# Performance work log

Hardware: AMD Instinct MI355X
Metric: run time of the kernel (lower is better)

The kernel has to match this reference:

```python
import jax, jax.numpy as jnp
import numpy as np

ITERS = 10
EPS = 1e-6
TEMPERATURE = 1.0


def setup_inputs() -> dict:
    key = jax.random.key(0)
    S, E = 524288, 64
    logits = jax.random.normal(key, (S, E), dtype=jnp.float32)
    return {"logits": logits, "top_k": 2}


def reference(logits, top_k):
    s, e = logits.shape
    scores = (logits / TEMPERATURE).astype(jnp.float32)
    scores = scores - jnp.max(scores, axis=-1, keepdims=True)
    q = jnp.exp(scores)
    col_target = float(s) / float(max(e, 1))

    def body(q, _):
        q = q / (jnp.sum(q, axis=1, keepdims=True) + EPS)
        q = q / (jnp.sum(q, axis=0, keepdims=True) + EPS) * col_target
        return q, None

    q, _ = jax.lax.scan(body, q, None, length=ITERS)
    q = q / (jnp.sum(q, axis=1, keepdims=True) + EPS)
    vals, idx = jax.lax.top_k(q, top_k)
    w = vals / (jnp.sum(vals, axis=-1, keepdims=True) + EPS)
    return idx.astype(jnp.int64), w.astype(logits.dtype)
```

## Files before the change

kernel.cpp:

```cpp
#include <hip/hip_runtime.h>
#include <math.h>

#define EPS 1e-6f
#define NE 64
#define TPB 1024
#define WPB 16
#define NBLK 256
#define NWAVES (NBLK * WPB)
#define ITERS 10
#define PF 4

template <int ctrl>
__device__ __forceinline__ float dppf(float x) {
    return __int_as_float(__builtin_amdgcn_update_dpp(
        0, __float_as_int(x), ctrl, 0xf, 0xf, true));
}
template <int ctrl>
__device__ __forceinline__ int dppi(int x) {
    return __builtin_amdgcn_update_dpp(0, x, ctrl, 0xf, 0xf, true);
}

__device__ __forceinline__ float group16_sum(float v) {
    v += dppf<0xB1>(v);
    v += dppf<0x4E>(v);
    v += dppf<0x141>(v);
    v += dppf<0x140>(v);
    return v;
}

#define ARGMAX_STEP(CTRL)                                      \
    {                                                          \
        float ov = dppf<CTRL>(v);                              \
        int oi = dppi<CTRL>(i);                                \
        if (ov > v || (ov == v && oi < i)) { v = ov; i = oi; } \
    }

__device__ __forceinline__ void group16_argmax(float& v, int& i) {
    ARGMAX_STEP(0xB1)
    ARGMAX_STEP(0x4E)
    ARGMAX_STEP(0x141)
    ARGMAX_STEP(0x140)
}

template <bool FIRST>
__global__ __launch_bounds__(TPB) void sink_pass(
    const float4* __restrict__ logits4, float* __restrict__ r,
    float* __restrict__ c, float* __restrict__ Pblk,
    unsigned* __restrict__ counters, int nquads, float col_target, int it) {
    const int tid = threadIdx.x;
    const int lane = tid & 63;
    const int wib = tid >> 6;
    const int g = lane >> 4;
    const int h = lane & 15;
    const int qpw = nquads / NWAVES;
    const int qbase = (blockIdx.x * WPB + wib) * qpw;

    float4 c4;
    if (FIRST) c4 = make_float4(1.f, 1.f, 1.f, 1.f);
    else       c4 = ((const float4*)c)[h];

    const float4* lp = logits4 + (size_t)qbase * 64 + lane;

    float4 buf[PF];
    float rbuf[PF];
#pragma unroll
    for (int p = 0; p < PF; ++p) buf[p] = lp[(size_t)p * 64];
    if (!FIRST) {
#pragma unroll
        for (int p = 0; p < PF; ++p) rbuf[p] = r[(qbase + p) * 4 + g];
    }

    float4 pacc = {0.f, 0.f, 0.f, 0.f};
    const int nb = qpw / PF;
    for (int b = 0; b < nb; ++b) {
        float4 cur[PF];
        float rcur[PF];
#pragma unroll
        for (int p = 0; p < PF; ++p) {
            cur[p] = buf[p];
            if (!FIRST) rcur[p] = rbuf[p];
        }
        if (b + 1 < nb) {
            const float4* np = lp + (size_t)(b + 1) * PF * 64;
#pragma unroll
            for (int p = 0; p < PF; ++p) buf[p] = np[(size_t)p * 64];
            if (!FIRST) {
#pragma unroll
                for (int p = 0; p < PF; ++p)
                    rbuf[p] = r[(qbase + (b + 1) * PF + p) * 4 + g];
            }
        }
#pragma unroll
        for (int p = 0; p < PF; ++p) {
            float4 q;
            q.x = __expf(cur[p].x); q.y = __expf(cur[p].y);
            q.z = __expf(cur[p].z); q.w = __expf(cur[p].w);
            float s = q.x * c4.x + q.y * c4.y + q.z * c4.z + q.w * c4.w;
            s = group16_sum(s);
            float rold = FIRST ? 1.0f : rcur[p];
            float rnew = rold / (rold * s + EPS);
            int row = (qbase + b * PF + p) * 4 + g;
            if (h == 0) r[row] = rnew;
            pacc.x += q.x * rnew; pacc.y += q.y * rnew;
            pacc.z += q.z * rnew; pacc.w += q.w * rnew;
        }
    }

    __shared__ float4 plds[WPB][64];
    __shared__ int lastflag;
    plds[wib][lane] = pacc;
    __syncthreads();
    if (tid < NE) {
        int j = tid, hh = j >> 2, kk = j & 3;
        float t = 0.f;
#pragma unroll
        for (int w = 0; w < WPB; ++w)
#pragma unroll
            for (int gg = 0; gg < 4; ++gg)
                t += ((const float*)&plds[w][gg * 16 + hh])[kk];
        Pblk[blockIdx.x * NE + j] = t;
        __threadfence();
    }
    __syncthreads();
    if (tid == 0) {
        unsigned old = atomicAdd(&counters[it], 1u);
        lastflag = (old == (unsigned)(NBLK - 1));
    }
    __syncthreads();

    if (lastflag) {
        __threadfence();
        float* s_red = (float*)plds;
        const int j = tid & 63;
        const int chunk = tid >> 6;
        float t = 0.f;
        int b0 = chunk * (NBLK / 16);
        for (int b = b0; b < b0 + NBLK / 16; ++b) t += Pblk[b * NE + j];
        __syncthreads();
        s_red[chunk * NE + j] = t;
        __syncthreads();
        if (tid < NE) {
            float P = 0.f;
#pragma unroll
            for (int k = 0; k < 16; ++k) P += s_red[k * NE + tid];
            float cj = FIRST ? 1.0f : c[tid];
            c[tid] = cj * col_target / (cj * P + EPS);
            __threadfence();
        }
    }
}

__global__ __launch_bounds__(TPB) void sink_final(
    const float4* __restrict__ logits4, const float* __restrict__ r,
    const float* __restrict__ c, float2* __restrict__ oidx,
    float2* __restrict__ ow, int nquads) {
    const int tid = threadIdx.x;
    const int lane = tid & 63;
    const int wib = tid >> 6;
    const int g = lane >> 4;
    const int h = lane & 15;
    const int base_col = h * 4;
    const int qpw = nquads / NWAVES;
    const int qbase = (blockIdx.x * WPB + wib) * qpw;

    const float4 c4 = ((const float4*)c)[h];
    const float4* lp = logits4 + (size_t)qbase * 64 + lane;

    float4 buf[PF];
    float rbuf[PF];
#pragma unroll
    for (int p = 0; p < PF; ++p) buf[p] = lp[(size_t)p * 64];
#pragma unroll
    for (int p = 0; p < PF; ++p) rbuf[p] = r[(qbase + p) * 4 + g];

    const int nb = qpw / PF;
    for (int b = 0; b < nb; ++b) {
        float4 cur[PF];
        float rcur[PF];
#pragma unroll
        for (int p = 0; p < PF; ++p) { cur[p] = buf[p]; rcur[p] = rbuf[p]; }
        if (b + 1 < nb) {
            const float4* np = lp + (size_t)(b + 1) * PF * 64;
#pragma unroll
            for (int p = 0; p < PF; ++p) buf[p] = np[(size_t)p * 64];
#pragma unroll
            for (int p = 0; p < PF; ++p)
                rbuf[p] = r[(qbase + (b + 1) * PF + p) * 4 + g];
        }
#pragma unroll
        for (int p = 0; p < PF; ++p) {
            float4 u;
            u.x = __expf(cur[p].x) * c4.x; u.y = __expf(cur[p].y) * c4.y;
            u.z = __expf(cur[p].z) * c4.z; u.w = __expf(cur[p].w) * c4.w;
            float s = group16_sum(u.x + u.y + u.z + u.w);
            float rold = rcur[p];
            float rnew = rold / (rold * s + EPS);
            float4 val;
            val.x = u.x * rnew; val.y = u.y * rnew;
            val.z = u.z * rnew; val.w = u.w * rnew;

            float v = val.x; int i = base_col;
            if (val.y > v) { v = val.y; i = base_col + 1; }
            if (val.z > v) { v = val.z; i = base_col + 2; }
            if (val.w > v) { v = val.w; i = base_col + 3; }
            group16_argmax(v, i);
            float v1 = v; int i1 = i;

            float4 mv;
            mv.x = (i1 == base_col)     ? -INFINITY : val.x;
            mv.y = (i1 == base_col + 1) ? -INFINITY : val.y;
            mv.z = (i1 == base_col + 2) ? -INFINITY : val.z;
            mv.w = (i1 == base_col + 3) ? -INFINITY : val.w;
            v = mv.x; i = base_col;
            if (mv.y > v) { v = mv.y; i = base_col + 1; }
            if (mv.z > v) { v = mv.z; i = base_col + 2; }
            if (mv.w > v) { v = mv.w; i = base_col + 3; }
            group16_argmax(v, i);
            float v2 = v; int i2 = i;

            if (h == 0) {
                int row = (qbase + b * PF + p) * 4 + g;
                float wsum = v1 + v2 + EPS;
                oidx[row] = make_float2((float)i1, (float)i2);
                ow[row] = make_float2(v1 / wsum, v2 / wsum);
            }
        }
    }
}

extern "C" void kernel_launch(void* const* d_in, const int* in_sizes, int n_in,
                              void* d_out, int out_size, void* d_ws, size_t ws_size,
                              hipStream_t stream) {
    const float* logits = (const float*)d_in[0];
    const int S = in_sizes[0] / NE;
    const int nquads = S / 4;
    const float col_target = (float)S / (float)NE;

    float* r = (float*)d_ws;
    float* c = r + S;
    float* Pblk = c + NE;
    unsigned* counters = (unsigned*)(Pblk + NBLK * NE);

    float* out = (float*)d_out;
    float2* oidx = (float2*)out;
    float2* ow = (float2*)(out + (size_t)2 * S);

    const float4* l4 = (const float4*)logits;

    hipMemsetAsync(counters, 0, ITERS * sizeof(unsigned), stream);
    sink_pass<true><<<NBLK, TPB, 0, stream>>>(l4, r, c, Pblk, counters,
                                              nquads, col_target, 0);
    for (int it = 1; it < ITERS; ++it)
        sink_pass<false><<<NBLK, TPB, 0, stream>>>(l4, r, c, Pblk, counters,
                                                   nquads, col_target, it);
    sink_final<<<NBLK, TPB, 0, stream>>>(l4, r, c, oidx, ow, nquads);
}
```

Measured before the change: 554.6 us.

## Fuse all Sinkhorn passes into one cooperative persistent kernel with grid barriers

Replaces the eleven separate kernel launches with a single cooperative kernel. Blocks synchronize between iterations through an atomic counter grid barrier and keep row scales in LDS instead of global memory, while column scales live in shared memory and are recomputed redundantly by every block. This removes launch gaps, the last-block serialization and the global traffic for row scales. In exchange it adds spin-wait barriers and relies on all 256 blocks being co-resident. MAXR=2048 must be large enough to hold the rows each block owns.

Result: slower. 1.236 ms (+122.9%).

```diff
diff --git a/kernel.cpp b/kernel.cpp
--- a/kernel.cpp
+++ b/kernel.cpp
@@ -9,6 +9,7 @@
 #define NWAVES (NBLK * WPB)
 #define ITERS 10
 #define PF 4
+#define MAXR 2048
 
 template <int ctrl>
 __device__ __forceinline__ float dppf(float x) {
@@ -42,11 +43,10 @@
     ARGMAX_STEP(0x140)
 }
 
-template <bool FIRST>
-__global__ __launch_bounds__(TPB) void sink_pass(
-    const float4* __restrict__ logits4, float* __restrict__ r,
-    float* __restrict__ c, float* __restrict__ Pblk,
-    unsigned* __restrict__ counters, int nquads, float col_target, int it) {
+__global__ __launch_bounds__(TPB, 1) void sink_all(
+    const float4* __restrict__ logits4, float* __restrict__ Pblk,
+    unsigned* __restrict__ counters, float2* __restrict__ oidx,
+    float2* __restrict__ ow, int nquads, float col_target) {
     const int tid = threadIdx.x;
     const int lane = tid & 63;
     const int wib = tid >> 6;
@@ -54,138 +54,117 @@
     const int h = lane & 15;
     const int qpw = nquads / NWAVES;
     const int qbase = (blockIdx.x * WPB + wib) * qpw;
+    const int nb = qpw / PF;
+
+    __shared__ float s_r[MAXR];
+    __shared__ float s_c[NE];
+    __shared__ float4 plds[WPB][64];
+    float* s_red = (float*)plds;
+
+    for (int i = tid; i < MAXR; i += TPB) s_r[i] = 1.0f;
+    if (tid < NE) s_c[tid] = 1.0f;
+    __syncthreads();
+
+    const float4* lp = logits4 + (size_t)qbase * 64 + lane;
+
+    for (int it = 0; it < ITERS; ++it) {
+        float4 c4;
+        c4.x = s_c[h * 4 + 0]; c4.y = s_c[h * 4 + 1];
+        c4.z = s_c[h * 4 + 2]; c4.w = s_c[h * 4 + 3];
+
+        float4 pacc = {0.f, 0.f, 0.f, 0.f};
+        float4 buf[PF];
+#pragma unroll
+        for (int p = 0; p < PF; ++p) buf[p] = lp[(size_t)p * 64];
+        for (int b = 0; b < nb; ++b) {
+            float4 cur[PF];
+#pragma unroll
+            for (int p = 0; p < PF; ++p) cur[p] = buf[p];
+            if (b + 1 < nb) {
+                const float4* np = lp + (size_t)(b + 1) * PF * 64;
+#pragma unroll
+                for (int p = 0; p < PF; ++p) buf[p] = np[(size_t)p * 64];
+            }
+#pragma unroll
+            for (int p = 0; p < PF; ++p) {
+                float4 q;
+                q.x = __expf(cur[p].x); q.y = __expf(cur[p].y);
+                q.z = __expf(cur[p].z); q.w = __expf(cur[p].w);
+                float s = q.x * c4.x + q.y * c4.y + q.z * c4.z + q.w * c4.w;
+                s = group16_sum(s);
+                int lrow = (wib * qpw + b * PF + p) * 4 + g;
+                float rold = s_r[lrow];
+                float rnew = rold / (rold * s + EPS);
+                if (h == 0) s_r[lrow] = rnew;
+                pacc.x += q.x * rnew; pacc.y += q.y * rnew;
+                pacc.z += q.z * rnew; pacc.w += q.w * rnew;
+            }
+        }
+
+        __syncthreads();
+        plds[wib][lane] = pacc;
+        __syncthreads();
+        float* Pout = Pblk + (size_t)((it & 1) * NBLK + blockIdx.x) * NE;
+        if (tid < NE) {
+            int j = tid, hh = j >> 2, kk = j & 3;
+            float t = 0.f;
+#pragma unroll
+            for (int w = 0; w < WPB; ++w)
+#pragma unroll
+                for (int gg = 0; gg < 4; ++gg)
+                    t += ((const float*)&plds[w][gg * 16 + hh])[kk];
+            Pout[j] = t;
+            __threadfence();
+        }
+        __syncthreads();
+        if (tid == 0) {
+            __hip_atomic_fetch_add(&counters[it], 1u, __ATOMIC_RELEASE,
+                                   __HIP_MEMORY_SCOPE_AGENT);
+            while (__hip_atomic_load(&counters[it], __ATOMIC_ACQUIRE,
+                                     __HIP_MEMORY_SCOPE_AGENT) !=
+                   (unsigned)NBLK)
+                __builtin_amdgcn_s_sleep(8);
+        }
+        __syncthreads();
+        __threadfence();
+
+        const float* Pin = Pblk + (size_t)(it & 1) * NBLK * NE;
+        {
+            const int j = tid & 63;
+            const int chunk = tid >> 6;
+            float t = 0.f;
+            int b0 = chunk * (NBLK / 16);
+            for (int b = b0; b < b0 + NBLK / 16; ++b) t += Pin[b * NE + j];
+            __syncthreads();
+            s_red[chunk * NE + j] = t;
+            __syncthreads();
+            if (tid < NE) {
+                float P = 0.f;
+#pragma unroll
+                for (int k = 0; k < 16; ++k) P += s_red[k * NE + tid];
+                float cj = s_c[tid];
+                s_c[tid] = cj * col_target / (cj * P + EPS);
+            }
+            __syncthreads();
+        }
+    }
 
     float4 c4;
-    if (FIRST) c4 = make_float4(1.f, 1.f, 1.f, 1.f);
-    else       c4 = ((const float4*)c)[h];
-
-    const float4* lp = logits4 + (size_t)qbase * 64 + lane;
+    c4.x = s_c[h * 4 + 0]; c4.y = s_c[h * 4 + 1];
+    c4.z = s_c[h * 4 + 2]; c4.w = s_c[h * 4 + 3];
+    const int base_col = h * 4;
 
     float4 buf[PF];
-    float rbuf[PF];
 #pragma unroll
     for (int p = 0; p < PF; ++p) buf[p] = lp[(size_t)p * 64];
-    if (!FIRST) {
-#pragma unroll
-        for (int p = 0; p < PF; ++p) rbuf[p] = r[(qbase + p) * 4 + g];
-    }
-
-    float4 pacc = {0.f, 0.f, 0.f, 0.f};
-    const int nb = qpw / PF;
     for (int b = 0; b < nb; ++b) {
         float4 cur[PF];
-        float rcur[PF];
-#pragma unroll
-        for (int p = 0; p < PF; ++p) {
-            cur[p] = buf[p];
-            if (!FIRST) rcur[p] = rbuf[p];
-        }
+#pragma unroll
+        for (int p = 0; p < PF; ++p) cur[p] = buf[p];
         if (b + 1 < nb) {
             const float4* np = lp + (size_t)(b + 1) * PF * 64;
 #pragma unroll
             for (int p = 0; p < PF; ++p) buf[p] = np[(size_t)p * 64];
-            if (!FIRST) {
-#pragma unroll
-                for (int p = 0; p < PF; ++p)
-                    rbuf[p] = r[(qbase + (b + 1) * PF + p) * 4 + g];
-            }
-        }
-#pragma unroll
-        for (int p = 0; p < PF; ++p) {
-            float4 q;
-            q.x = __expf(cur[p].x); q.y = __expf(cur[p].y);
-            q.z = __expf(cur[p].z); q.w = __expf(cur[p].w);
-            float s = q.x * c4.x + q.y * c4.y + q.z * c4.z + q.w * c4.w;
-            s = group16_sum(s);
-            float rold = FIRST ? 1.0f : rcur[p];
-            float rnew = rold / (rold * s + EPS);
-            int row = (qbase + b * PF + p) * 4 + g;
-            if (h == 0) r[row] = rnew;
-            pacc.x += q.x * rnew; pacc.y += q.y * rnew;
-            pacc.z += q.z * rnew; pacc.w += q.w * rnew;
-        }
-    }
-
-    __shared__ float4 plds[WPB][64];
-    __shared__ int lastflag;
-    plds[wib][lane] = pacc;
-    __syncthreads();
-    if (tid < NE) {
-        int j = tid, hh = j >> 2, kk = j & 3;
-        float t = 0.f;
-#pragma unroll
-        for (int w = 0; w < WPB; ++w)
-#pragma unroll
-            for (int gg = 0; gg < 4; ++gg)
-                t += ((const float*)&plds[w][gg * 16 + hh])[kk];
-        Pblk[blockIdx.x * NE + j] = t;
-        __threadfence();
-    }
-    __syncthreads();
-    if (tid == 0) {
-        unsigned old = atomicAdd(&counters[it], 1u);
-        lastflag = (old == (unsigned)(NBLK - 1));
-    }
-    __syncthreads();
-
-    if (lastflag) {
-        __threadfence();
-        float* s_red = (float*)plds;
-        const int j = tid & 63;
-        const int chunk = tid >> 6;
-        float t = 0.f;
-        int b0 = chunk * (NBLK / 16);
-        for (int b = b0; b < b0 + NBLK / 16; ++b) t += Pblk[b * NE + j];
-        __syncthreads();
-        s_red[chunk * NE + j] = t;
-        __syncthreads();
-        if (tid < NE) {
-            float P = 0.f;
-#pragma unroll
-            for (int k = 0; k < 16; ++k) P += s_red[k * NE + tid];
-            float cj = FIRST ? 1.0f : c[tid];
-            c[tid] = cj * col_target / (cj * P + EPS);
-            __threadfence();
-        }
-    }
-}
-
-__global__ __launch_bounds__(TPB) void sink_final(
-    const float4* __restrict__ logits4, const float* __restrict__ r,
-    const float* __restrict__ c, float2* __restrict__ oidx,
-    float2* __restrict__ ow, int nquads) {
-    const int tid = threadIdx.x;
-    const int lane = tid & 63;
-    const int wib = tid >> 6;
-    const int g = lane >> 4;
-    const int h = lane & 15;
-    const int base_col = h * 4;
-    const int qpw = nquads / NWAVES;
-    const int qbase = (blockIdx.x * WPB + wib) * qpw;
-
-    const float4 c4 = ((const float4*)c)[h];
-    const float4* lp = logits4 + (size_t)qbase * 64 + lane;
-
-    float4 buf[PF];
-    float rbuf[PF];
-#pragma unroll
-    for (int p = 0; p < PF; ++p) buf[p] = lp[(size_t)p * 64];
-#pragma unroll
-    for (int p = 0; p < PF; ++p) rbuf[p] = r[(qbase + p) * 4 + g];
-
-    const int nb = qpw / PF;
-    for (int b = 0; b < nb; ++b) {
-        float4 cur[PF];
-        float rcur[PF];
-#pragma unroll
-        for (int p = 0; p < PF; ++p) { cur[p] = buf[p]; rcur[p] = rbuf[p]; }
-        if (b + 1 < nb) {
-            const float4* np = lp + (size_t)(b + 1) * PF * 64;
-#pragma unroll
-            for (int p = 0; p < PF; ++p) buf[p] = np[(size_t)p * 64];
-#pragma unroll
-            for (int p = 0; p < PF; ++p)
-                rbuf[p] = r[(qbase + (b + 1) * PF + p) * 4 + g];
         }
 #pragma unroll
         for (int p = 0; p < PF; ++p) {
@@ -193,7 +172,8 @@
             u.x = __expf(cur[p].x) * c4.x; u.y = __expf(cur[p].y) * c4.y;
             u.z = __expf(cur[p].z) * c4.z; u.w = __expf(cur[p].w) * c4.w;
             float s = group16_sum(u.x + u.y + u.z + u.w);
-            float rold = rcur[p];
+            int lrow = (wib * qpw + b * PF + p) * 4 + g;
+            float rold = s_r[lrow];
             float rnew = rold / (rold * s + EPS);
             float4 val;
             val.x = u.x * rnew; val.y = u.y * rnew;
@@ -233,13 +213,11 @@
                               hipStream_t stream) {
     const float* logits = (const float*)d_in[0];
     const int S = in_sizes[0] / NE;
-    const int nquads = S / 4;
-    const float col_target = (float)S / (float)NE;
-
-    float* r = (float*)d_ws;
-    float* c = r + S;
-    float* Pblk = c + NE;
-    unsigned* counters = (unsigned*)(Pblk + NBLK * NE);
+    int nquads = S / 4;
+    float col_target = (float)S / (float)NE;
+
+    float* Pblk = (float*)d_ws;
+    unsigned* counters = (unsigned*)(Pblk + 2 * NBLK * NE);
 
     float* out = (float*)d_out;
     float2* oidx = (float2*)out;
@@ -248,10 +226,8 @@
     const float4* l4 = (const float4*)logits;
 
     hipMemsetAsync(counters, 0, ITERS * sizeof(unsigned), stream);
-    sink_pass<true><<<NBLK, TPB, 0, stream>>>(l4, r, c, Pblk, counters,
-                                              nquads, col_target, 0);
-    for (int it = 1; it < ITERS; ++it)
-        sink_pass<false><<<NBLK, TPB, 0, stream>>>(l4, r, c, Pblk, counters,
-                                                   nquads, col_target, it);
-    sink_final<<<NBLK, TPB, 0, stream>>>(l4, r, c, oidx, ow, nquads);
-}
+    void* args[] = {(void*)&l4, (void*)&Pblk, (void*)&counters, (void*)&oidx,
+                    (void*)&ow, (void*)&nquads, (void*)&col_target};
+    hipLaunchCooperativeKernel((void*)sink_all, dim3(NBLK), dim3(TPB), args,
+                               0, stream);
+}
```
